# Kernel tuning notes

Hardware: AMD Instinct MI355X
Metric: run time of the kernel (lower is better)

Reference implementation:

```python
import jax, jax.numpy as jnp
import numpy as np

IN_DIM = 128
DIM = 32
N_HEADS = 4
LN_EPS = 1e-5


def setup_inputs() -> dict:
    key = jax.random.key(0)
    ks = jax.random.split(key, 10)
    B, N = 1, 256
    z = jax.random.normal(ks[0], (B, N, N, IN_DIM), dtype=jnp.float32)
    src_mask = jax.random.randint(ks[1], (B, N), 0, 2, dtype=jnp.int32)
    s = 1.0 / np.sqrt(IN_DIM)
    # weights stored in (in, out) layout: y = x @ W + b
    return {
        "z": z,
        "src_mask": src_mask,
        "ln_g": jnp.ones((IN_DIM,), jnp.float32),
        "ln_b": jnp.zeros((IN_DIM,), jnp.float32),
        "w_qkv": jax.random.normal(ks[2], (IN_DIM, 3 * N_HEADS * DIM), jnp.float32) * s,
        "w_pair": jax.random.normal(ks[3], (IN_DIM, N_HEADS), jnp.float32) * s,
        "w_gate": jax.random.normal(ks[4], (IN_DIM, IN_DIM), jnp.float32) * s,
        "b_gate": jnp.zeros((IN_DIM,), jnp.float32),
        "w_out": jax.random.normal(ks[5], (N_HEADS * DIM, IN_DIM), jnp.float32) * s,
        "b_out": jnp.zeros((IN_DIM,), jnp.float32),
    }


def reference(z, src_mask, ln_g, ln_b, w_qkv, w_pair, w_gate, b_gate, w_out, b_out):
    B, N, _, _ = z.shape
    H, D = N_HEADS, DIM
    # src_mask: zeros -> -1 (as in the torch in-place assignment)
    m = jnp.where(src_mask == 0, -1.0, 1.0).astype(z.dtype)  # [B, N]
    attn_mask = m[:, :, None] * m[:, None, :]                # [B, N, N], -1 where exactly one is masked
    # LayerNorm over last dim
    mu = jnp.mean(z, axis=-1, keepdims=True)
    var = jnp.mean(jnp.square(z - mu), axis=-1, keepdims=True)
    zn = (z - mu) / jnp.sqrt(var + LN_EPS) * ln_g + ln_b
    # QKV projection (no bias)
    qkv = zn @ w_qkv                                         # [B, N, N, 3*H*D]
    q, k, v = jnp.split(qkv, 3, axis=-1)
    q = q.reshape(B, N, N, H, D)
    k = k.reshape(B, N, N, H, D)
    v = v.reshape(B, N, N, H, D)
    pb = zn @ w_pair                                         # [B, N, N, H] pair bias
    gate = jax.nn.sigmoid(zn @ w_gate + b_gate)              # [B, N, N, IN_DIM]
    scale = float(np.sqrt(D))
    # row-wise triangle attention: attend over j within each row r
    logits = jnp.einsum('brihd,brjhd->brijh', q, k) / scale  # [B, N(r), N(i), N(j), H]
    logits = logits + pb[:, None, :, :, :]                   # bias broadcast over r
    # faithful to torch: masked positions set to -1e-9 (not -inf)
    logits = jnp.where(attn_mask[:, None, :, :, None] == -1, jnp.asarray(-1e-9, logits.dtype), logits)
    attn = jax.nn.softmax(logits, axis=3)
    out = jnp.einsum('brijh,brjhd->brihd', attn, v)          # [B, N, N, H, D]
    out = gate * out.reshape(B, N, N, H * D)
    return out @ w_out + b_out
```

## Files before the change

### kernel.cpp

```cpp
#include <hip/hip_runtime.h>
#include <hip/hip_bf16.h>
#include <math.h>


#define NPOS 65536
#define LN_EPS 1e-5f
#define SCALE_L2E 0.25503487f
#define MASKVAL  -1.4426950e-9f

typedef __attribute__((ext_vector_type(8))) short bf16x8;
typedef __attribute__((ext_vector_type(4))) float f32x4;

__device__ __forceinline__ short f2b(float f) {
    union { float f; unsigned u; } c; c.f = f;
    unsigned r = c.u + 0x7FFFu + ((c.u >> 16) & 1u);
    return (short)(r >> 16);
}
__device__ __forceinline__ unsigned cvt_pk(float lo, float hi) {
    unsigned r;
    asm("v_cvt_pk_bf16_f32 %0, %1, %2" : "=v"(r) : "v"(lo), "v"(hi));
    return r;
}
__device__ __forceinline__ float b2f_lo(unsigned u) {
    union { unsigned u; float f; } c; c.u = u << 16; return c.f;
}
__device__ __forceinline__ float b2f_hi(unsigned u) {
    union { unsigned u; float f; } c; c.u = u & 0xFFFF0000u; return c.f;
}

__global__ void k_prep(const float* __restrict__ wq, const float* __restrict__ wg,
                       const float* __restrict__ wp, const float* __restrict__ wo,
                       const int* __restrict__ smask,
                       short* __restrict__ wT, short* __restrict__ woT,
                       unsigned* __restrict__ mjbg)
{
    const int idx = blockIdx.x * 256 + threadIdx.x;
    const int stride = gridDim.x * 256;
    for (int i = idx; i < 528 * 128; i += stride) {
        const int o = i >> 7, c = i & 127;
        float v;
        if (o < 384)      v = wq[c * 384 + o];
        else if (o < 512) v = wg[c * 128 + (o - 384)];
        else if (o < 516) v = wp[c * 4 + (o - 512)] * 1.4426950408889634f;
        else              v = 0.f;
        wT[i] = f2b(v);
    }
    for (int i = idx; i < 128 * 128; i += stride) {
        const int o = i >> 7, c = i & 127;
        woT[i] = f2b(wo[c * 128 + o]);
    }
    if (blockIdx.x == 0 && threadIdx.x < 8) {
        const int gr = threadIdx.x >> 1, hw = threadIdx.x & 1;
        unsigned wbits = 0;
        for (int b = 0; b < 32; ++b) {
            const int k = hw * 32 + b;
            const int j = (k >> 2) * 16 + gr * 4 + (k & 3);
            if (smask[j] == 0) wbits |= (1u << b);
        }
        mjbg[threadIdx.x] = wbits;
    }
}

__global__ __launch_bounds__(256) void k_proj(
    const float* __restrict__ z, const float* __restrict__ ln_g,
    const float* __restrict__ ln_b, const short* __restrict__ wT,
    const float* __restrict__ b_gate, short* __restrict__ qkb,
    short* __restrict__ Vtb, short* __restrict__ pbb, short* __restrict__ gate_b)
{
    __shared__ short sBuf[17920];
    const int t = threadIdx.x, w = t >> 6, l = t & 63;
    const int lg = l & 15, gr = l >> 4;
    const int p0 = blockIdx.x * 64;
    const f32x4 zero4 = {0.f, 0.f, 0.f, 0.f};
    short* sV = sBuf;
    short* sG = sBuf + 9216;

    {
        const int row = t >> 2, q = t & 3;
        const float* zr = z + (size_t)(p0 + row) * 128 + q * 32;
        float v[32];
        float s = 0.f, sq = 0.f;
#pragma unroll
        for (int u = 0; u < 8; ++u) {
            const float4 f = ((const float4*)zr)[u];
            v[u * 4 + 0] = f.x; v[u * 4 + 1] = f.y;
            v[u * 4 + 2] = f.z; v[u * 4 + 3] = f.w;
            s += f.x + f.y + f.z + f.w;
            sq += f.x * f.x + f.y * f.y + f.z * f.z + f.w * f.w;
        }
        s  += __shfl_xor(s, 1, 4);  s  += __shfl_xor(s, 2, 4);
        sq += __shfl_xor(sq, 1, 4); sq += __shfl_xor(sq, 2, 4);
        const float mu = s * (1.f / 128.f);
        const float rstd = rsqrtf(sq * (1.f / 128.f) - mu * mu + LN_EPS);
        short tmp[32];
#pragma unroll
        for (int u = 0; u < 32; ++u) {
            const int c = q * 32 + u;
            tmp[u] = f2b((v[u] - mu) * rstd * ln_g[c] + ln_b[c]);
        }
        uint4* dst = (uint4*)(sBuf + row * 264 + q * 32);
#pragma unroll
        for (int u = 0; u < 4; ++u) dst[u] = *(uint4*)&tmp[u * 8];
    }
    __syncthreads();

    bf16x8 a[4][4];
#pragma unroll
    for (int mt = 0; mt < 4; ++mt)
#pragma unroll
        for (int kc = 0; kc < 4; ++kc)
            a[mt][kc] = *(const bf16x8*)(sBuf + (mt * 16 + lg) * 264 + kc * 32 + gr * 8);
    __syncthreads();

    for (int nt = w; nt < 16; nt += 4) {
        bf16x8 bfr[4];
#pragma unroll
        for (int kc = 0; kc < 4; ++kc)
            bfr[kc] = *(const bf16x8*)(wT + (size_t)(nt * 16 + lg) * 128 + kc * 32 + gr * 8);
        const int o = nt * 16 + lg;
#pragma unroll
        for (int mt = 0; mt < 4; ++mt) {
            f32x4 acc = zero4;
#pragma unroll
            for (int kc = 0; kc < 4; ++kc)
                acc = __builtin_amdgcn_mfma_f32_16x16x32_bf16(a[mt][kc], bfr[kc], acc, 0, 0, 0);
#pragma unroll
            for (int reg = 0; reg < 4; ++reg)
                sBuf[(mt * 16 + gr * 4 + reg) * 264 + o] = f2b(acc[reg]);
        }
    }
    __syncthreads();
    {
        const int row = t >> 2, seg = t & 3;
        const short* src = sBuf + row * 264 + seg * 64;
        short* dst = qkb + (size_t)(p0 + row) * 256 + seg * 64;
#pragma unroll
        for (int u = 0; u < 8; ++u)
            *(uint4*)(dst + u * 8) = *(const uint4*)(src + u * 8);
    }
    __syncthreads();

    for (int nt = 16 + w; nt < 33; nt += 4) {
        bf16x8 bfr[4];
#pragma unroll
        for (int kc = 0; kc < 4; ++kc)
            bfr[kc] = *(const bf16x8*)(wT + (size_t)(nt * 16 + lg) * 128 + kc * 32 + gr * 8);
        const int o = nt * 16 + lg;
#pragma unroll
        for (int mt = 0; mt < 4; ++mt) {
            f32x4 acc = zero4;
#pragma unroll
            for (int kc = 0; kc < 4; ++kc)
                acc = __builtin_amdgcn_mfma_f32_16x16x32_bf16(a[mt][kc], bfr[kc], acc, 0, 0, 0);
            const int pr = p0 + mt * 16 + gr * 4;
            if (o < 384) {
                const int row = o - 256;
                const int jl = mt * 16 + gr * 4;
                const int jp = (jl & 0x23) | ((jl & 12) << 1) | ((jl >> 2) & 4);
                union { unsigned long long u; short sh[4]; } pk;
#pragma unroll
                for (int reg = 0; reg < 4; ++reg) pk.sh[reg] = f2b(acc[reg]);
                *(unsigned long long*)(sV + row * 72 + jp) = pk.u;
            } else if (o < 512) {
                const int c = o - 384;
                const float bg = b_gate[c];
#pragma unroll
                for (int reg = 0; reg < 4; ++reg)
                    sG[(mt * 16 + gr * 4 + reg) * 136 + c] =
                        f2b(1.f / (1.f + __expf(-(acc[reg] + bg))));
            } else if (o < 516) {
                union { unsigned long long u; short sh[4]; } pk;
#pragma unroll
                for (int reg = 0; reg < 4; ++reg) pk.sh[reg] = f2b(acc[reg]);
                *(unsigned long long*)(pbb + (size_t)(o - 512) * NPOS + pr) = pk.u;
            }
        }
    }
    __syncthreads();

    {
        const int r = p0 >> 8, jbase = p0 & 255;
        const int row = t >> 1, half = t & 1;
        const short* src = sV + row * 72 + half * 32;
        const int hh = row >> 5, d = row & 31;
        short* dst = Vtb + (((size_t)hh * 256 + r) * 32 + d) * 256 + jbase + half * 32;
#pragma unroll
        for (int u = 0; u < 4; ++u)
            *(uint4*)(dst + u * 8) = *(const uint4*)(src + u * 8);

        const int grow = t >> 2, q = t & 3;
        const short* gsrc = sG + grow * 136 + q * 32;
        short* gdst = gate_b + (size_t)(p0 + grow) * 128 + q * 32;
#pragma unroll
        for (int u = 0; u < 4; ++u)
            *(uint4*)(gdst + u * 8) = *(const uint4*)(gsrc + u * 8);
    }
}

__global__ __launch_bounds__(256, 4) void k_attn(
    const short* __restrict__ qkb, const short* __restrict__ Vtb,
    const short* __restrict__ pbb, const int* __restrict__ smask,
    const short* __restrict__ gate_b, const unsigned* __restrict__ mjbg,
    short* __restrict__ aob)
{
    __shared__ short sK[8192];
    __shared__ short sV[8192];
    const int t = threadIdx.x, wv = t >> 6, l = t & 63;
    const int lg = l & 15, gr = l >> 4;
    const int bid = blockIdx.x;
    const int r = (bid & 7) * 32 + (bid >> 5);
    const int h = (bid >> 3) & 3;
    const int rb = r * 256;
    const f32x4 zero4 = {0.f, 0.f, 0.f, 0.f};
    const unsigned long long mjb = ((const unsigned long long*)mjbg)[gr];
    bf16x8 ones;
#pragma unroll
    for (int u = 0; u < 8; ++u) ones[u] = (short)0x3F80;

#pragma unroll
    for (int it = 0; it < 4; ++it) {
        const int chunk = it * 256 + t;
        const int j = chunk >> 2, dg = chunk & 3;
        const uint4 v = *(const uint4*)(qkb + (size_t)(rb + j) * 256 + 128 + h * 32 + dg * 8);
        *(uint4*)(sK + (((j >> 4) * 4 + dg) * 16 + (j & 15)) * 8) = v;
    }
#pragma unroll
    for (int it = 0; it < 4; ++it) {
        const int d = it * 8 + (t >> 5), kcgr = t & 31;
        const uint4 v = *(const uint4*)(Vtb + (((size_t)h * 256 + r) * 32 + d) * 256 + kcgr * 8);
        *(uint4*)(sV + (kcgr * 32 + (d ^ (kcgr & 7))) * 8) = v;
    }
    __syncthreads();

    for (int tl = 0; tl < 4; ++tl) {
        const int i0 = wv * 64 + tl * 16;
        const bf16x8 qf = *(const bf16x8*)(qkb + (size_t)(rb + i0 + lg) * 256 + h * 32 + gr * 8);
        const bool bi = smask[i0 + lg] == 0;
        const short* pbrow = pbb + (size_t)h * NPOS + (size_t)(i0 + lg) * 256;

        f32x4 o0 = zero4, o1 = zero4, o2 = zero4;

        unsigned pkA[16];
#pragma unroll
        for (int nt = 0; nt < 8; ++nt) {
            const bf16x8 kf = *(const bf16x8*)(sK + ((nt * 4 + gr) * 16 + lg) * 8);
            const uint2 pbp = *(const uint2*)(pbrow + nt * 16 + gr * 4);
            const f32x4 s4 = __builtin_amdgcn_mfma_f32_16x16x32_bf16(kf, qf, zero4, 0, 0, 0);
            const float pbv[4] = { b2f_lo(pbp.x), b2f_hi(pbp.x), b2f_lo(pbp.y), b2f_hi(pbp.y) };
            float pv[4];
#pragma unroll
            for (int reg = 0; reg < 4; ++reg) {
                const bool bj = (mjb >> (nt * 4 + reg)) & 1;
                float lv = fmaf(s4[reg], SCALE_L2E, pbv[reg]);
                lv = (bi != bj) ? MASKVAL : lv;
                pv[reg] = exp2f(lv);
            }
            pkA[nt * 2 + 0] = cvt_pk(pv[0], pv[1]);
            pkA[nt * 2 + 1] = cvt_pk(pv[2], pv[3]);
        }
        __builtin_amdgcn_s_setprio(1);
#pragma unroll
        for (int kc = 0; kc < 4; ++kc) {
            const int kcgr = kc * 4 + gr, c7 = kcgr & 7;
            const bf16x8 pa = *(const bf16x8*)(&pkA[kc * 4]);
            const bf16x8 v0 = *(const bf16x8*)(sV + (kcgr * 32 + (lg ^ c7)) * 8);
            const bf16x8 v1 = *(const bf16x8*)(sV + (kcgr * 32 + 16 + (lg ^ c7)) * 8);
            o0 = __builtin_amdgcn_mfma_f32_16x16x32_bf16(pa, v0, o0, 0, 0, 0);
            o1 = __builtin_amdgcn_mfma_f32_16x16x32_bf16(pa, v1, o1, 0, 0, 0);
            o2 = __builtin_amdgcn_mfma_f32_16x16x32_bf16(pa, ones, o2, 0, 0, 0);
        }
        __builtin_amdgcn_s_setprio(0);

        unsigned pkB[16];
#pragma unroll
        for (int nt = 8; nt < 16; ++nt) {
            const bf16x8 kf = *(const bf16x8*)(sK + ((nt * 4 + gr) * 16 + lg) * 8);
            const uint2 pbp = *(const uint2*)(pbrow + nt * 16 + gr * 4);
            const f32x4 s4 = __builtin_amdgcn_mfma_f32_16x16x32_bf16(kf, qf, zero4, 0, 0, 0);
            const float pbv[4] = { b2f_lo(pbp.x), b2f_hi(pbp.x), b2f_lo(pbp.y), b2f_hi(pbp.y) };
            float pv[4];
#pragma unroll
            for (int reg = 0; reg < 4; ++reg) {
                const bool bj = (mjb >> (nt * 4 + reg)) & 1;
                float lv = fmaf(s4[reg], SCALE_L2E, pbv[reg]);
                lv = (bi != bj) ? MASKVAL : lv;
                pv[reg] = exp2f(lv);
            }
            pkB[(nt - 8) * 2 + 0] = cvt_pk(pv[0], pv[1]);
            pkB[(nt - 8) * 2 + 1] = cvt_pk(pv[2], pv[3]);
        }
        __builtin_amdgcn_s_setprio(1);
#pragma unroll
        for (int kc = 4; kc < 8; ++kc) {
            const int kcgr = kc * 4 + gr, c7 = kcgr & 7;
            const bf16x8 pa = *(const bf16x8*)(&pkB[(kc - 4) * 4]);
            const bf16x8 v0 = *(const bf16x8*)(sV + (kcgr * 32 + (lg ^ c7)) * 8);
            const bf16x8 v1 = *(const bf16x8*)(sV + (kcgr * 32 + 16 + (lg ^ c7)) * 8);
            o0 = __builtin_amdgcn_mfma_f32_16x16x32_bf16(pa, v0, o0, 0, 0, 0);
            o1 = __builtin_amdgcn_mfma_f32_16x16x32_bf16(pa, v1, o1, 0, 0, 0);
            o2 = __builtin_amdgcn_mfma_f32_16x16x32_bf16(pa, ones, o2, 0, 0, 0);
        }
        __builtin_amdgcn_s_setprio(0);

#pragma unroll
        for (int reg = 0; reg < 4; ++reg) {
            const int p = rb + i0 + gr * 4 + reg;
            const float g0 = b2f_lo((unsigned)*(const unsigned short*)(gate_b + (size_t)p * 128 + h * 32 + lg));
            const float g1 = b2f_lo((unsigned)*(const unsigned short*)(gate_b + (size_t)p * 128 + h * 32 + 16 + lg));
            const float inv = 1.f / o2[reg];
            short* dst = aob + ((size_t)h * NPOS + p) * 32;
            dst[lg]      = f2b(o0[reg] * inv * g0);
            dst[16 + lg] = f2b(o1[reg] * inv * g1);
        }
    }
}

__global__ __launch_bounds__(256) void k_out(
    const short* __restrict__ aob, const short* __restrict__ woT,
    const float* __restrict__ b_out, float* __restrict__ out)
{
    const int t = threadIdx.x, w = t >> 6, l = t & 63;
    const int lg = l & 15, gr = l >> 4;
    const int p0 = blockIdx.x * 64;
    const f32x4 zero4 = {0.f, 0.f, 0.f, 0.f};

    bf16x8 a[4][4];
#pragma unroll
    for (int mt = 0; mt < 4; ++mt)
#pragma unroll
        for (int kc = 0; kc < 4; ++kc)
            a[mt][kc] = *(const bf16x8*)(aob + ((size_t)kc * NPOS + p0 + mt * 16 + lg) * 32 + gr * 8);

    for (int nt = w; nt < 8; nt += 4) {
        bf16x8 bw[4];
#pragma unroll
        for (int kc = 0; kc < 4; ++kc)
            bw[kc] = *(const bf16x8*)(woT + (size_t)(nt * 16 + lg) * 128 + kc * 32 + gr * 8);
        const int o = nt * 16 + lg;
        const float bo = b_out[o];
#pragma unroll
        for (int mt = 0; mt < 4; ++mt) {
            f32x4 c = zero4;
#pragma unroll
            for (int kc = 0; kc < 4; ++kc)
                c = __builtin_amdgcn_mfma_f32_16x16x32_bf16(a[mt][kc], bw[kc], c, 0, 0, 0);
#pragma unroll
            for (int reg = 0; reg < 4; ++reg)
                out[(size_t)(p0 + mt * 16 + gr * 4 + reg) * 128 + o] = c[reg] + bo;
        }
    }
}

extern "C" void kernel_launch(void* const* d_in, const int* in_sizes, int n_in,
                              void* d_out, int out_size, void* d_ws, size_t ws_size,
                              hipStream_t stream)
{
    const float* z      = (const float*)d_in[0];
    const int*   smask  = (const int*)d_in[1];
    const float* ln_g   = (const float*)d_in[2];
    const float* ln_b   = (const float*)d_in[3];
    const float* w_qkv  = (const float*)d_in[4];
    const float* w_pair = (const float*)d_in[5];
    const float* w_gate = (const float*)d_in[6];
    const float* b_gate = (const float*)d_in[7];
    const float* w_out  = (const float*)d_in[8];
    const float* b_out  = (const float*)d_in[9];
    float* out = (float*)d_out;

    short* ws      = (short*)d_ws;
    short* qkb     = ws;
    short* Vtb     = qkb + (size_t)NPOS * 256;
    short* wT      = Vtb + (size_t)8388608;
    short* woT     = wT + 528 * 128;
    unsigned* mjbg = (unsigned*)(woT + 128 * 128);
    short* pbb     = (short*)(mjbg + 16);
    short* gate_b  = pbb + (size_t)4 * NPOS;
    short* aob     = gate_b + (size_t)NPOS * 128;

    k_prep<<<64, 256, 0, stream>>>(w_qkv, w_gate, w_pair, w_out, smask, wT, woT, mjbg);
    k_proj<<<NPOS / 64, 256, 0, stream>>>(z, ln_g, ln_b, wT, b_gate, qkb, Vtb, pbb, gate_b);
    k_attn<<<1024, 256, 0, stream>>>(qkb, Vtb, pbb, smask, gate_b, mjbg, aob);
    k_out<<<NPOS / 64, 256, 0, stream>>>(aob, woT, b_out, out);
}
```

Before: 110.8 us.

## Store gate channel-major and pack bf16 conversions in projection kernel

Gate values are now written channel-major (gate_c[c][pos]) via a transposed shared tile, so the attention epilogue can load four consecutive positions' gates with a single 8-byte read per channel instead of scattered 2-byte loads. The projection kernel also swaps MFMA operand order so QK results are stored as packed 4-element rows, uses the hardware packed bf16 convert instead of manual rounding, and rotates the copy-out segment per row to spread LDS bank accesses. The intent is to cut global and LDS access overhead. The trade-off is a less contiguous store pattern for the gate in k_proj, and b2f_hi must exist in the hidden helper code.

```diff
diff --git a/kernel.cpp b/kernel.cpp
--- a/kernel.cpp
+++ b/kernel.cpp
@@ -65,7 +65,7 @@
     const float* __restrict__ z, const float* __restrict__ ln_g,
     const float* __restrict__ ln_b, const short* __restrict__ wT,
     const float* __restrict__ b_gate, short* __restrict__ qkb,
-    short* __restrict__ Vtb, short* __restrict__ pbb, short* __restrict__ gate_b)
+    short* __restrict__ Vtb, short* __restrict__ pbb, short* __restrict__ gate_c)
 {
     __shared__ short sBuf[17920];
     const int t = threadIdx.x, w = t >> 6, l = t & 63;
@@ -73,7 +73,7 @@
     const int p0 = blockIdx.x * 64;
     const f32x4 zero4 = {0.f, 0.f, 0.f, 0.f};
     short* sV = sBuf;
-    short* sG = sBuf + 9216;
+    short* sGt = sBuf + 9216;
 
     {
         const int row = t >> 2, q = t & 3;
@@ -92,15 +92,17 @@
         sq += __shfl_xor(sq, 1, 4); sq += __shfl_xor(sq, 2, 4);
         const float mu = s * (1.f / 128.f);
         const float rstd = rsqrtf(sq * (1.f / 128.f) - mu * mu + LN_EPS);
-        short tmp[32];
-#pragma unroll
-        for (int u = 0; u < 32; ++u) {
-            const int c = q * 32 + u;
-            tmp[u] = f2b((v[u] - mu) * rstd * ln_g[c] + ln_b[c]);
+        unsigned tmp32[16];
+#pragma unroll
+        for (int u = 0; u < 16; ++u) {
+            const int c = q * 32 + u * 2;
+            const float a0 = (v[u * 2] - mu) * rstd * ln_g[c] + ln_b[c];
+            const float a1 = (v[u * 2 + 1] - mu) * rstd * ln_g[c + 1] + ln_b[c + 1];
+            tmp32[u] = cvt_pk(a0, a1);
         }
         uint4* dst = (uint4*)(sBuf + row * 264 + q * 32);
 #pragma unroll
-        for (int u = 0; u < 4; ++u) dst[u] = *(uint4*)&tmp[u * 8];
+        for (int u = 0; u < 4; ++u) dst[u] = *(uint4*)&tmp32[u * 4];
     }
     __syncthreads();
 
@@ -117,23 +119,23 @@
 #pragma unroll
         for (int kc = 0; kc < 4; ++kc)
             bfr[kc] = *(const bf16x8*)(wT + (size_t)(nt * 16 + lg) * 128 + kc * 32 + gr * 8);
-        const int o = nt * 16 + lg;
 #pragma unroll
         for (int mt = 0; mt < 4; ++mt) {
             f32x4 acc = zero4;
 #pragma unroll
             for (int kc = 0; kc < 4; ++kc)
-                acc = __builtin_amdgcn_mfma_f32_16x16x32_bf16(a[mt][kc], bfr[kc], acc, 0, 0, 0);
-#pragma unroll
-            for (int reg = 0; reg < 4; ++reg)
-                sBuf[(mt * 16 + gr * 4 + reg) * 264 + o] = f2b(acc[reg]);
+                acc = __builtin_amdgcn_mfma_f32_16x16x32_bf16(bfr[kc], a[mt][kc], acc, 0, 0, 0);
+            uint2 pk;
+            pk.x = cvt_pk(acc[0], acc[1]);
+            pk.y = cvt_pk(acc[2], acc[3]);
+            *(uint2*)(sBuf + (mt * 16 + lg) * 264 + nt * 16 + gr * 4) = pk;
         }
     }
     __syncthreads();
     {
-        const int row = t >> 2, seg = t & 3;
-        const short* src = sBuf + row * 264 + seg * 64;
-        short* dst = qkb + (size_t)(p0 + row) * 256 + seg * 64;
+        const int row = t >> 2, rot = (t + row) & 3;
+        const short* src = sBuf + row * 264 + rot * 64;
+        short* dst = qkb + (size_t)(p0 + row) * 256 + rot * 64;
 #pragma unroll
         for (int u = 0; u < 8; ++u)
             *(uint4*)(dst + u * 8) = *(const uint4*)(src + u * 8);
@@ -157,22 +159,26 @@
                 const int row = o - 256;
                 const int jl = mt * 16 + gr * 4;
                 const int jp = (jl & 0x23) | ((jl & 12) << 1) | ((jl >> 2) & 4);
-                union { unsigned long long u; short sh[4]; } pk;
-#pragma unroll
-                for (int reg = 0; reg < 4; ++reg) pk.sh[reg] = f2b(acc[reg]);
-                *(unsigned long long*)(sV + row * 72 + jp) = pk.u;
+                uint2 pk;
+                pk.x = cvt_pk(acc[0], acc[1]);
+                pk.y = cvt_pk(acc[2], acc[3]);
+                *(uint2*)(sV + row * 72 + jp) = pk;
             } else if (o < 512) {
                 const int c = o - 384;
                 const float bg = b_gate[c];
+                float gv[4];
 #pragma unroll
                 for (int reg = 0; reg < 4; ++reg)
-                    sG[(mt * 16 + gr * 4 + reg) * 136 + c] =
-                        f2b(1.f / (1.f + __expf(-(acc[reg] + bg))));
+                    gv[reg] = 1.f / (1.f + __expf(-(acc[reg] + bg)));
+                uint2 pk;
+                pk.x = cvt_pk(gv[0], gv[1]);
+                pk.y = cvt_pk(gv[2], gv[3]);
+                *(uint2*)(sGt + c * 68 + mt * 16 + gr * 4) = pk;
             } else if (o < 516) {
-                union { unsigned long long u; short sh[4]; } pk;
-#pragma unroll
-                for (int reg = 0; reg < 4; ++reg) pk.sh[reg] = f2b(acc[reg]);
-                *(unsigned long long*)(pbb + (size_t)(o - 512) * NPOS + pr) = pk.u;
+                uint2 pk;
+                pk.x = cvt_pk(acc[0], acc[1]);
+                pk.y = cvt_pk(acc[2], acc[3]);
+                *(uint2*)(pbb + (size_t)(o - 512) * NPOS + pr) = pk;
             }
         }
     }
@@ -188,19 +194,19 @@
         for (int u = 0; u < 4; ++u)
             *(uint4*)(dst + u * 8) = *(const uint4*)(src + u * 8);
 
-        const int grow = t >> 2, q = t & 3;
-        const short* gsrc = sG + grow * 136 + q * 32;
-        short* gdst = gate_b + (size_t)(p0 + grow) * 128 + q * 32;
-#pragma unroll
-        for (int u = 0; u < 4; ++u)
-            *(uint4*)(gdst + u * 8) = *(const uint4*)(gsrc + u * 8);
+        const int c = t >> 1;
+        const short* gsrc = sGt + c * 68 + half * 32;
+        short* gdst = gate_c + (size_t)c * NPOS + p0 + half * 32;
+#pragma unroll
+        for (int u = 0; u < 8; ++u)
+            *(uint2*)(gdst + u * 4) = *(const uint2*)(gsrc + u * 4);
     }
 }
 
 __global__ __launch_bounds__(256, 4) void k_attn(
     const short* __restrict__ qkb, const short* __restrict__ Vtb,
     const short* __restrict__ pbb, const int* __restrict__ smask,
-    const short* __restrict__ gate_b, const unsigned* __restrict__ mjbg,
+    const short* __restrict__ gate_c, const unsigned* __restrict__ mjbg,
     short* __restrict__ aob)
 {
     __shared__ short sK[8192];
@@ -302,11 +308,15 @@
         }
         __builtin_amdgcn_s_setprio(0);
 
+        const uint2 gu0 = *(const uint2*)(gate_c + (size_t)(h * 32 + lg) * NPOS + rb + i0 + gr * 4);
+        const uint2 gu1 = *(const uint2*)(gate_c + (size_t)(h * 32 + 16 + lg) * NPOS + rb + i0 + gr * 4);
 #pragma unroll
         for (int reg = 0; reg < 4; ++reg) {
             const int p = rb + i0 + gr * 4 + reg;
-            const float g0 = b2f_lo((unsigned)*(const unsigned short*)(gate_b + (size_t)p * 128 + h * 32 + lg));
-            const float g1 = b2f_lo((unsigned)*(const unsigned short*)(gate_b + (size_t)p * 128 + h * 32 + 16 + lg));
+            const unsigned w0 = (reg < 2) ? gu0.x : gu0.y;
+            const unsigned w1 = (reg < 2) ? gu1.x : gu1.y;
+            const float g0 = (reg & 1) ? b2f_hi(w0) : b2f_lo(w0);
+            const float g1 = (reg & 1) ? b2f_hi(w1) : b2f_lo(w1);
             const float inv = 1.f / o2[reg];
             short* dst = aob + ((size_t)h * NPOS + p) * 32;
             dst[lg]      = f2b(o0[reg] * inv * g0);
@@ -374,11 +384,11 @@
     short* woT     = wT + 528 * 128;
     unsigned* mjbg = (unsigned*)(woT + 128 * 128);
     short* pbb     = (short*)(mjbg + 16);
-    short* gate_b  = pbb + (size_t)4 * NPOS;
-    short* aob     = gate_b + (size_t)NPOS * 128;
+    short* gate_c  = pbb + (size_t)4 * NPOS;
+    short* aob     = gate_c + (size_t)128 * NPOS;
 
     k_prep<<<64, 256, 0, stream>>>(w_qkv, w_gate, w_pair, w_out, smask, wT, woT, mjbg);
-    k_proj<<<NPOS / 64, 256, 0, stream>>>(z, ln_g, ln_b, wT, b_gate, qkb, Vtb, pbb, gate_b);
-    k_attn<<<1024, 256, 0, stream>>>(qkb, Vtb, pbb, smask, gate_b, mjbg, aob);
+    k_proj<<<NPOS / 64, 256, 0, stream>>>(z, ln_g, ln_b, wT, b_gate, qkb, Vtb, pbb, gate_c);
+    k_attn<<<1024, 256, 0, stream>>>(qkb, Vtb, pbb, smask, gate_c, mjbg, aob);
     k_out<<<NPOS / 64, 256, 0, stream>>>(aob, woT, b_out, out);
 }
```

New measurement: 114.2 us. 3.1% more time.

## Write Q/K in MFMA-fragment tiled layout directly from registers, skip LDS staging

Applied to the files above, without the earlier changes.

The Q/K projection in k_proj now swaps the MFMA operand order and stores each 16x16 output tile straight to global memory in a per-block fragment-tiled layout (qkbT), packed with v_cvt_pk_bf16_f32. This removes the LDS round trip, the scalar bf16 stores, the coalesced copy-out and two barriers. k_attn is changed to read Q and K fragments from the new layout using two 8-byte loads each. The LDS buffer is shrunk to a 136-stride region shared by normalized z and the gate, and k_proj gains an occupancy hint of 4 blocks via launch bounds. The trade-off is narrower global stores and loads in place of 16-byte ones.

```diff
diff --git a/kernel.cpp b/kernel.cpp
--- a/kernel.cpp
+++ b/kernel.cpp
@@ -61,10 +61,10 @@
     }
 }
 
-__global__ __launch_bounds__(256) void k_proj(
+__global__ __launch_bounds__(256, 4) void k_proj(
     const float* __restrict__ z, const float* __restrict__ ln_g,
     const float* __restrict__ ln_b, const short* __restrict__ wT,
-    const float* __restrict__ b_gate, short* __restrict__ qkb,
+    const float* __restrict__ b_gate, short* __restrict__ qkbT,
     short* __restrict__ Vtb, short* __restrict__ pbb, short* __restrict__ gate_b)
 {
     __shared__ short sBuf[17920];
@@ -73,7 +73,7 @@
     const int p0 = blockIdx.x * 64;
     const f32x4 zero4 = {0.f, 0.f, 0.f, 0.f};
     short* sV = sBuf;
-    short* sG = sBuf + 9216;
+    short* sZn = sBuf + 9216;
 
     {
         const int row = t >> 2, q = t & 3;
@@ -98,7 +98,7 @@
             const int c = q * 32 + u;
             tmp[u] = f2b((v[u] - mu) * rstd * ln_g[c] + ln_b[c]);
         }
-        uint4* dst = (uint4*)(sBuf + row * 264 + q * 32);
+        uint4* dst = (uint4*)(sZn + row * 136 + q * 32);
 #pragma unroll
         for (int u = 0; u < 4; ++u) dst[u] = *(uint4*)&tmp[u * 8];
     }
@@ -109,36 +109,27 @@
     for (int mt = 0; mt < 4; ++mt)
 #pragma unroll
         for (int kc = 0; kc < 4; ++kc)
-            a[mt][kc] = *(const bf16x8*)(sBuf + (mt * 16 + lg) * 264 + kc * 32 + gr * 8);
+            a[mt][kc] = *(const bf16x8*)(sZn + (mt * 16 + lg) * 136 + kc * 32 + gr * 8);
     __syncthreads();
 
+    short* qblk = qkbT + (size_t)blockIdx.x * 16384;
     for (int nt = w; nt < 16; nt += 4) {
         bf16x8 bfr[4];
 #pragma unroll
         for (int kc = 0; kc < 4; ++kc)
             bfr[kc] = *(const bf16x8*)(wT + (size_t)(nt * 16 + lg) * 128 + kc * 32 + gr * 8);
-        const int o = nt * 16 + lg;
 #pragma unroll
         for (int mt = 0; mt < 4; ++mt) {
             f32x4 acc = zero4;
 #pragma unroll
             for (int kc = 0; kc < 4; ++kc)
-                acc = __builtin_amdgcn_mfma_f32_16x16x32_bf16(a[mt][kc], bfr[kc], acc, 0, 0, 0);
-#pragma unroll
-            for (int reg = 0; reg < 4; ++reg)
-                sBuf[(mt * 16 + gr * 4 + reg) * 264 + o] = f2b(acc[reg]);
-        }
-    }
-    __syncthreads();
-    {
-        const int row = t >> 2, seg = t & 3;
-        const short* src = sBuf + row * 264 + seg * 64;
-        short* dst = qkb + (size_t)(p0 + row) * 256 + seg * 64;
-#pragma unroll
-        for (int u = 0; u < 8; ++u)
-            *(uint4*)(dst + u * 8) = *(const uint4*)(src + u * 8);
-    }
-    __syncthreads();
+                acc = __builtin_amdgcn_mfma_f32_16x16x32_bf16(bfr[kc], a[mt][kc], acc, 0, 0, 0);
+            uint2 pk;
+            pk.x = cvt_pk(acc[0], acc[1]);
+            pk.y = cvt_pk(acc[2], acc[3]);
+            *(uint2*)(qblk + (nt * 4 + mt) * 256 + gr * 64 + lg * 4) = pk;
+        }
+    }
 
     for (int nt = 16 + w; nt < 33; nt += 4) {
         bf16x8 bfr[4];
@@ -166,7 +157,7 @@
                 const float bg = b_gate[c];
 #pragma unroll
                 for (int reg = 0; reg < 4; ++reg)
-                    sG[(mt * 16 + gr * 4 + reg) * 136 + c] =
+                    sZn[(mt * 16 + gr * 4 + reg) * 136 + c] =
                         f2b(1.f / (1.f + __expf(-(acc[reg] + bg))));
             } else if (o < 516) {
                 union { unsigned long long u; short sh[4]; } pk;
@@ -189,7 +180,7 @@
             *(uint4*)(dst + u * 8) = *(const uint4*)(src + u * 8);
 
         const int grow = t >> 2, q = t & 3;
-        const short* gsrc = sG + grow * 136 + q * 32;
+        const short* gsrc = sZn + grow * 136 + q * 32;
         short* gdst = gate_b + (size_t)(p0 + grow) * 128 + q * 32;
 #pragma unroll
         for (int u = 0; u < 4; ++u)
@@ -198,7 +189,7 @@
 }
 
 __global__ __launch_bounds__(256, 4) void k_attn(
-    const short* __restrict__ qkb, const short* __restrict__ Vtb,
+    const short* __restrict__ qkbT, const short* __restrict__ Vtb,
     const short* __restrict__ pbb, const int* __restrict__ smask,
     const short* __restrict__ gate_b, const unsigned* __restrict__ mjbg,
     short* __restrict__ aob)
@@ -221,7 +212,12 @@
     for (int it = 0; it < 4; ++it) {
         const int chunk = it * 256 + t;
         const int j = chunk >> 2, dg = chunk & 3;
-        const uint4 v = *(const uint4*)(qkb + (size_t)(rb + j) * 256 + 128 + h * 32 + dg * 8);
+        const short* kb = qkbT + ((size_t)(r * 4 + (j >> 6))) * 16384
+                        + ((8 + h * 2 + (dg >> 1)) * 4 + ((j >> 4) & 3)) * 256
+                        + ((dg & 1) * 2) * 64 + (j & 15) * 4;
+        uint4 v;
+        { const uint2 lo = *(const uint2*)kb, hi = *(const uint2*)(kb + 64);
+          v.x = lo.x; v.y = lo.y; v.z = hi.x; v.w = hi.y; }
         *(uint4*)(sK + (((j >> 4) * 4 + dg) * 16 + (j & 15)) * 8) = v;
     }
 #pragma unroll
@@ -234,7 +230,16 @@
 
     for (int tl = 0; tl < 4; ++tl) {
         const int i0 = wv * 64 + tl * 16;
-        const bf16x8 qf = *(const bf16x8*)(qkb + (size_t)(rb + i0 + lg) * 256 + h * 32 + gr * 8);
+        bf16x8 qf;
+        {
+            const short* qb = qkbT + ((size_t)(r * 4 + wv)) * 16384
+                            + ((h * 2 + (gr >> 1)) * 4 + tl) * 256
+                            + ((gr & 1) * 2) * 64 + lg * 4;
+            union { bf16x8 v; uint2 u2[2]; } qu;
+            qu.u2[0] = *(const uint2*)qb;
+            qu.u2[1] = *(const uint2*)(qb + 64);
+            qf = qu.v;
+        }
         const bool bi = smask[i0 + lg] == 0;
         const short* pbrow = pbb + (size_t)h * NPOS + (size_t)(i0 + lg) * 256;
 
@@ -368,8 +373,8 @@
     float* out = (float*)d_out;
 
     short* ws      = (short*)d_ws;
-    short* qkb     = ws;
-    short* Vtb     = qkb + (size_t)NPOS * 256;
+    short* qkbT    = ws;
+    short* Vtb     = qkbT + (size_t)NPOS * 256;
     short* wT      = Vtb + (size_t)8388608;
     short* woT     = wT + 528 * 128;
     unsigned* mjbg = (unsigned*)(woT + 128 * 128);
@@ -378,7 +383,7 @@
     short* aob     = gate_b + (size_t)NPOS * 128;
 
     k_prep<<<64, 256, 0, stream>>>(w_qkv, w_gate, w_pair, w_out, smask, wT, woT, mjbg);
-    k_proj<<<NPOS / 64, 256, 0, stream>>>(z, ln_g, ln_b, wT, b_gate, qkb, Vtb, pbb, gate_b);
-    k_attn<<<1024, 256, 0, stream>>>(qkb, Vtb, pbb, smask, gate_b, mjbg, aob);
+    k_proj<<<NPOS / 64, 256, 0, stream>>>(z, ln_g, ln_b, wT, b_gate, qkbT, Vtb, pbb, gate_b);
+    k_attn<<<1024, 256, 0, stream>>>(qkbT, Vtb, pbb, smask, gate_b, mjbg, aob);
     k_out<<<NPOS / 64, 256, 0, stream>>>(aob, woT, b_out, out);
 }
```

Result: faster. 104.4 us (-5.8%).
